# Performance work log

Measured on AMD Instinct MI355X. Metric: run time of the kernel, lower is better.

The kernel has to match this reference:

```python
import jax, jax.numpy as jnp
import numpy as np

BETA_MIN, BETA_MAX = 0.01, 0.995
EPS_DELTA, EPS_RMS = 1e-6, 1e-5


def _rmsnorm(x, w):
    ms = jnp.mean(x * x, axis=-1, keepdims=True)
    return x * jax.lax.rsqrt(ms + EPS_RMS) * w


def _delta_scan(q, k, v, beta, mask, bb1, bb2):
    # q, k, v: [B, S, D]; beta, mask: [B, S, 1]; bb1, bb2: scalars
    phi_q = jax.nn.elu(q) + 1.0
    phi_k = jax.nn.elu(k) + 1.0
    b1_base = jnp.clip(jax.nn.sigmoid(bb1), BETA_MIN, BETA_MAX)
    b2_base = jnp.clip(jax.nn.sigmoid(bb2), BETA_MIN, BETA_MAX)
    B, S, D = q.shape

    def step(carry, inp):
        H1, H2, Z1, Z2 = carry
        qt, kt, vt, bt, mt = inp  # qt/kt/vt: [B,D], bt/mt: [B,1]
        bin_t = jnp.clip(bt, BETA_MIN, BETA_MAX)
        b1 = jnp.clip(b1_base * bin_t, BETA_MIN, BETA_MAX)  # [B,1]
        b2 = jnp.clip(b2_base * bin_t, BETA_MIN, BETA_MAX)
        kv = jnp.einsum('bd,be->bde', kt, vt) * mt[:, :, None]  # [B,D,D]
        H1 = H1 * b1[:, :, None] + kv
        H2 = H2 * b2[:, :, None] + kv
        km = kt * mt
        Z1 = Z1 * b1 + km
        Z2 = Z2 * b2 + km
        num = jnp.einsum('bd,bde->be', qt, H1 + H2)
        den = jnp.maximum(jnp.sum(qt * (Z1 + Z2), axis=-1, keepdims=True), EPS_DELTA)
        return (H1, H2, Z1, Z2), num / den * mt

    init = (jnp.zeros((B, D, D), q.dtype), jnp.zeros((B, D, D), q.dtype),
            jnp.zeros((B, D), q.dtype), jnp.zeros((B, D), q.dtype))
    xs = tuple(a.swapaxes(0, 1) for a in (phi_q, phi_k, v, beta, mask))
    _, outs = jax.lax.scan(step, init, xs)
    return outs.swapaxes(0, 1)  # [B, S, D]


def setup_inputs() -> dict:
    key = jax.random.key(0)
    B, S, Dm, H = 4, 2048, 512, 8
    ks = jax.random.split(key, 8)
    scale = float(1.0 / np.sqrt(Dm))
    return {
        'x': jax.random.normal(ks[0], (B, S, Dm), jnp.float32),
        'mask': jnp.ones((B, S), jnp.float32),
        'Wq': jax.random.normal(ks[1], (Dm, Dm), jnp.float32) * scale,
        'Wk': jax.random.normal(ks[2], (Dm, Dm), jnp.float32) * scale,
        'Wv': jax.random.normal(ks[3], (Dm, Dm), jnp.float32) * scale,
        'Wb': jax.random.normal(ks[4], (H, Dm), jnp.float32) * scale,
        'bb': jnp.full((H,), 1.5, jnp.float32),
        'Wo': jax.random.normal(ks[5], (Dm, Dm), jnp.float32) * scale,
        'bo': jnp.zeros((Dm,), jnp.float32),
        'ln_w': jnp.ones((Dm,), jnp.float32),
        'recency': jnp.zeros((H,), jnp.float32),
        'base_beta_1': jnp.asarray(2.0, jnp.float32),
        'base_beta_2': jnp.asarray(3.0, jnp.float32),
    }


def reference(x, mask, Wq, Wk, Wv, Wb, bb, Wo, bo, ln_w, recency,
              base_beta_1, base_beta_2):
    B, S, Dm = x.shape
    H = recency.shape[0]
    d = Dm // H
    h = _rmsnorm(x, ln_w)
    q = h @ Wq.T
    k = h @ Wk.T
    v = h @ Wv.T
    # input-conditioned gate with per-head recency bias  -> [B, S, H]
    beta = jax.nn.sigmoid(h @ Wb.T + bb + recency)

    def to_heads(t):  # [B,S,Dm] -> [B*H, S, d]
        return t.reshape(B, S, H, d).transpose(0, 2, 1, 3).reshape(B * H, S, d)

    qh, kh, vh = to_heads(q), to_heads(k), to_heads(v)
    betah = beta.transpose(0, 2, 1).reshape(B * H, S, 1)
    maskh = jnp.broadcast_to(mask[:, None, :, None], (B, H, S, 1)).reshape(B * H, S, 1)
    o = _delta_scan(qh, kh, vh, betah, maskh, base_beta_1, base_beta_2)
    o = o.reshape(B, H, S, d).transpose(0, 2, 1, 3).reshape(B, S, Dm)
    return x + (o @ Wo.T + bo)
```

## Files before the change

kernel.cpp:

```cpp
#include <hip/hip_runtime.h>
#include <stdint.h>

typedef unsigned short u16;
typedef short bf16x8 __attribute__((ext_vector_type(8)));
typedef unsigned short u16x8 __attribute__((ext_vector_type(8)));
typedef unsigned short u16x4 __attribute__((ext_vector_type(4)));
typedef float f32x4 __attribute__((ext_vector_type(4)));

#define S_ 2048
#define DM 512
#define DH 64
#define CL 64
#define NCH 32

#define SW(r, sc) ((r) * 72 + ((sc) ^ (((r) & 7) << 3)))

__device__ __forceinline__ float b2f(u16 u) { return __uint_as_float(((unsigned)u) << 16); }
__device__ __forceinline__ u16 f2b(float f) {
    unsigned v = __float_as_uint(f);
    unsigned r = v + 0x7fffu + ((v >> 16) & 1u);
    return (u16)(r >> 16);
}
__device__ __forceinline__ float phi_elu(float x) { return x > 0.f ? x + 1.f : __expf(x); }
__device__ __forceinline__ float clip01(float v) { return fminf(fmaxf(v, 0.01f), 0.995f); }

__global__ __launch_bounds__(256) void k_rmsnorm(const float* __restrict__ x,
                                                 const float* __restrict__ lnw,
                                                 u16* __restrict__ h) {
    int wave = threadIdx.x >> 6, lane = threadIdx.x & 63;
    int row = blockIdx.x * 4 + wave;
    const float* xr = x + (size_t)row * DM + lane * 8;
    float4 v0 = *(const float4*)xr;
    float4 v1 = *(const float4*)(xr + 4);
    float ss = v0.x * v0.x + v0.y * v0.y + v0.z * v0.z + v0.w * v0.w +
               v1.x * v1.x + v1.y * v1.y + v1.z * v1.z + v1.w * v1.w;
    #pragma unroll
    for (int off = 32; off; off >>= 1) ss += __shfl_xor(ss, off, 64);
    float sc = rsqrtf(ss * (1.f / DM) + 1e-5f);
    const float* wr_ = lnw + lane * 8;
    float4 w0 = *(const float4*)wr_;
    float4 w1 = *(const float4*)(wr_ + 4);
    u16x8 o;
    o[0] = f2b(v0.x * sc * w0.x); o[1] = f2b(v0.y * sc * w0.y);
    o[2] = f2b(v0.z * sc * w0.z); o[3] = f2b(v0.w * sc * w0.w);
    o[4] = f2b(v1.x * sc * w1.x); o[5] = f2b(v1.y * sc * w1.y);
    o[6] = f2b(v1.z * sc * w1.z); o[7] = f2b(v1.w * sc * w1.w);
    *(u16x8*)(h + (size_t)row * DM + lane * 8) = o;
}

__global__ __launch_bounds__(256) void k_convw(const float* __restrict__ Wq, const float* __restrict__ Wk,
                                               const float* __restrict__ Wv, const float* __restrict__ Wo,
                                               u16* __restrict__ wcat, u16* __restrict__ wo) {
    int idx = blockIdx.x * 256 + threadIdx.x;
    int e0 = idx << 2;
    if (e0 < 1536 * 512) {
        int r = e0 >> 9, ccol = e0 & 511;
        const float* src = (r < 512) ? (Wq + (size_t)r * 512)
                         : (r < 1024) ? (Wk + (size_t)(r - 512) * 512)
                                      : (Wv + (size_t)(r - 1024) * 512);
        float4 v = *(const float4*)(src + ccol);
        u16x4 o = {f2b(v.x), f2b(v.y), f2b(v.z), f2b(v.w)};
        *(u16x4*)(wcat + e0) = o;
    } else {
        int e = e0 - 1536 * 512;
        float4 v = *(const float4*)(Wo + e);
        u16x4 o = {f2b(v.x), f2b(v.y), f2b(v.z), f2b(v.w)};
        *(u16x4*)(wo + e) = o;
    }
}

template<int MODE>
__global__ __launch_bounds__(256) void k_gemm(const u16* __restrict__ A, const u16* __restrict__ Bw, int K,
                                              const float* __restrict__ mask, u16* __restrict__ qh,
                                              u16* __restrict__ kh, u16* __restrict__ vh,
                                              const float* __restrict__ xres, const float* __restrict__ bo,
                                              float* __restrict__ outp) {
    __shared__ u16 As[128 * 40];
    __shared__ u16 Bs[128 * 40];
    int tid = threadIdx.x;
    int lane = tid & 63, wave = tid >> 6;
    int wr = wave >> 1, wc = wave & 1;
    int m0 = blockIdx.x * 128, n0 = blockIdx.y * 128;
    f32x4 acc[4][4] = {};
    int srow = tid >> 2, sc8 = (tid & 3) << 3;
    const u16* Ag0 = A + (size_t)(m0 + srow) * K + sc8;
    const u16* Ag1 = Ag0 + (size_t)64 * K;
    const u16* Bg0 = Bw + (size_t)(n0 + srow) * K + sc8;
    const u16* Bg1 = Bg0 + (size_t)64 * K;
    u16* As0 = &As[srow * 40 + sc8];
    u16* As1 = &As[(srow + 64) * 40 + sc8];
    u16* Bs0 = &Bs[srow * 40 + sc8];
    u16* Bs1 = &Bs[(srow + 64) * 40 + sc8];
    int kh8 = (lane >> 4) << 3;
    for (int k0 = 0; k0 < K; k0 += 32) {
        u16x8 a0 = *(const u16x8*)(Ag0 + k0);
        u16x8 a1 = *(const u16x8*)(Ag1 + k0);
        u16x8 b0 = *(const u16x8*)(Bg0 + k0);
        u16x8 b1 = *(const u16x8*)(Bg1 + k0);
        if (k0) __syncthreads();
        *(u16x8*)As0 = a0; *(u16x8*)As1 = a1;
        *(u16x8*)Bs0 = b0; *(u16x8*)Bs1 = b1;
        __syncthreads();
        bf16x8 af[4], bfr[4];
        #pragma unroll
        for (int m = 0; m < 4; m++) af[m] = *(const bf16x8*)&As[(wr * 64 + m * 16 + (lane & 15)) * 40 + kh8];
        #pragma unroll
        for (int n = 0; n < 4; n++) bfr[n] = *(const bf16x8*)&Bs[(wc * 64 + n * 16 + (lane & 15)) * 40 + kh8];
        #pragma unroll
        for (int m = 0; m < 4; m++)
            #pragma unroll
            for (int n = 0; n < 4; n++)
                acc[m][n] = __builtin_amdgcn_mfma_f32_16x16x32_bf16(af[m], bfr[n], acc[m][n], 0, 0, 0);
    }
    #pragma unroll
    for (int m = 0; m < 4; m++) {
        int rbase = m0 + wr * 64 + m * 16 + ((lane >> 4) << 2);
        #pragma unroll
        for (int n = 0; n < 4; n++) {
            int col = n0 + wc * 64 + n * 16 + (lane & 15);
            #pragma unroll
            for (int r = 0; r < 4; r++) {
                int row = rbase + r;
                float v = acc[m][n][r];
                if constexpr (MODE == 0) {
                    int mat = col >> 9, f = col & 511, hh = f >> 6, j = f & 63;
                    int b = row >> 11, s = row & 2047;
                    size_t di = ((size_t)((b << 3) + hh) * S_ + s) * DH + j;
                    if (mat == 0) qh[di] = f2b(phi_elu(v));
                    else if (mat == 1) kh[di] = f2b(phi_elu(v) * mask[(b << 11) + s]);
                    else vh[di] = f2b(v);
                } else {
                    size_t oi = (size_t)row * DM + col;
                    outp[oi] = v + xres[oi] + bo[col];
                }
            }
        }
    }
}

__global__ __launch_bounds__(256) void k_beta(const u16* __restrict__ h, const float* __restrict__ Wb,
                                              const float* __restrict__ bb, const float* __restrict__ rec,
                                              const float* __restrict__ bb1p, const float* __restrict__ bb2p,
                                              float* __restrict__ lb1, float* __restrict__ lb2) {
    int wave = threadIdx.x >> 6, lane = threadIdx.x & 63;
    int row = blockIdx.x * 4 + wave;
    const u16* hr = h + (size_t)row * DM + lane * 8;
    u16x8 hu = *(const u16x8*)hr;
    float hv[8];
    #pragma unroll
    for (int j = 0; j < 8; j++) hv[j] = b2f(hu[j]);
    float acc[8];
    #pragma unroll
    for (int hd = 0; hd < 8; hd++) {
        const float* wp = Wb + hd * DM + lane * 8;
        float4 w0 = *(const float4*)wp;
        float4 w1 = *(const float4*)(wp + 4);
        acc[hd] = hv[0] * w0.x + hv[1] * w0.y + hv[2] * w0.z + hv[3] * w0.w +
                  hv[4] * w1.x + hv[5] * w1.y + hv[6] * w1.z + hv[7] * w1.w;
    }
    #pragma unroll
    for (int hd = 0; hd < 8; hd++) {
        #pragma unroll
        for (int off = 32; off; off >>= 1) acc[hd] += __shfl_xor(acc[hd], off, 64);
    }
    if (lane == 0) {
        float b1b = clip01(1.f / (1.f + __expf(-bb1p[0])));
        float b2b = clip01(1.f / (1.f + __expf(-bb2p[0])));
        int b = row >> 11, s = row & 2047;
        #pragma unroll
        for (int hd = 0; hd < 8; hd++) {
            float logit = acc[hd] + bb[hd] + rec[hd];
            float beta = 1.f / (1.f + __expf(-logit));
            float bin = clip01(beta);
            float b1 = clip01(b1b * bin);
            float b2 = clip01(b2b * bin);
            size_t o = (size_t)((b << 3) + hd) * S_ + s;
            lb1[o] = log2f(b1);
            lb2[o] = log2f(b2);
        }
    }
}

__global__ __launch_bounds__(256) void k_pass1(const u16* __restrict__ kh, const u16* __restrict__ vh,
                                               const float* __restrict__ lb1, const float* __restrict__ lb2,
                                               float* __restrict__ S1, float* __restrict__ S2,
                                               float* __restrict__ z1, float* __restrict__ z2,
                                               float* __restrict__ P1, float* __restrict__ P2) {
    __shared__ u16 Kw1[64 * 72];
    __shared__ u16 Kw2[64 * 72];
    __shared__ u16 Vt[64 * 72];
    __shared__ float Ls1[64], Ls2[64];
    int tid = threadIdx.x;
    int bh = blockIdx.x >> 5, c = blockIdx.x & 31;
    int wave = tid >> 6, lane = tid & 63;
    size_t base = ((size_t)bh * S_ + c * CL) * DH;
    if (wave == 0) {
        float v = lb1[(size_t)bh * S_ + c * CL + lane];
        #pragma unroll
        for (int d = 1; d < 64; d <<= 1) { float o = __shfl_up(v, d, 64); if (lane >= d) v += o; }
        Ls1[lane] = v;
    } else if (wave == 1) {
        float v = lb2[(size_t)bh * S_ + c * CL + lane];
        #pragma unroll
        for (int d = 1; d < 64; d <<= 1) { float o = __shfl_up(v, d, 64); if (lane >= d) v += o; }
        Ls2[lane] = v;
    }
    int ss = tid & 63, i0 = (tid >> 6) << 4;
    const u16* kr = kh + base + (size_t)ss * DH + i0;
    u16x8 kk0 = *(const u16x8*)kr;
    u16x8 kk1 = *(const u16x8*)(kr + 8);
    {
        const u16* vr = vh + base + (size_t)ss * DH + i0;
        u16x8 vv0 = *(const u16x8*)vr;
        u16x8 vv1 = *(const u16x8*)(vr + 8);
        #pragma unroll
        for (int j = 0; j < 8; j++) {
            Vt[SW(i0 + j, ss)] = vv0[j];
            Vt[SW(i0 + 8 + j, ss)] = vv1[j];
        }
    }
    __syncthreads();
    float w1 = exp2f(Ls1[63] - Ls1[ss]);
    float w2 = exp2f(Ls2[63] - Ls2[ss]);
    #pragma unroll
    for (int j = 0; j < 8; j++) {
        float k0 = b2f(kk0[j]), k1 = b2f(kk1[j]);
        Kw1[SW(i0 + j, ss)] = f2b(w1 * k0);
        Kw2[SW(i0 + j, ss)] = f2b(w2 * k0);
        Kw1[SW(i0 + 8 + j, ss)] = f2b(w1 * k1);
        Kw2[SW(i0 + 8 + j, ss)] = f2b(w2 * k1);
    }
    if (tid == 0) { P1[blockIdx.x] = exp2f(Ls1[63]); P2[blockIdx.x] = exp2f(Ls2[63]); }
    __syncthreads();
    int l15 = lane & 15, kh8 = (lane >> 4) << 3;
    int j0 = wave << 4;
    bf16x8 vf0 = *(const bf16x8*)&Vt[SW(j0 + l15, kh8)];
    bf16x8 vf1 = *(const bf16x8*)&Vt[SW(j0 + l15, 32 + kh8)];
    f32x4 a1[4], a2[4];
    #pragma unroll
    for (int it = 0; it < 4; it++) { a1[it] = (f32x4){0,0,0,0}; a2[it] = (f32x4){0,0,0,0}; }
    #pragma unroll
    for (int it = 0; it < 4; it++) {
        int ir = (it << 4) + l15;
        bf16x8 b0 = *(const bf16x8*)&Kw1[SW(ir, kh8)];
        bf16x8 b1 = *(const bf16x8*)&Kw1[SW(ir, 32 + kh8)];
        a1[it] = __builtin_amdgcn_mfma_f32_16x16x32_bf16(vf0, b0, a1[it], 0, 0, 0);
        a1[it] = __builtin_amdgcn_mfma_f32_16x16x32_bf16(vf1, b1, a1[it], 0, 0, 0);
        bf16x8 c0 = *(const bf16x8*)&Kw2[SW(ir, kh8)];
        bf16x8 c1 = *(const bf16x8*)&Kw2[SW(ir, 32 + kh8)];
        a2[it] = __builtin_amdgcn_mfma_f32_16x16x32_bf16(vf0, c0, a2[it], 0, 0, 0);
        a2[it] = __builtin_amdgcn_mfma_f32_16x16x32_bf16(vf1, c1, a2[it], 0, 0, 0);
    }
    {
        int iz = tid >> 2, sg = tid & 3;
        u16x8 x0 = *(const u16x8*)&Kw1[SW(iz, sg << 4)];
        u16x8 x1 = *(const u16x8*)&Kw1[SW(iz, (sg << 4) + 8)];
        u16x8 y0 = *(const u16x8*)&Kw2[SW(iz, sg << 4)];
        u16x8 y1 = *(const u16x8*)&Kw2[SW(iz, (sg << 4) + 8)];
        float z1v = 0.f, z2v = 0.f;
        #pragma unroll
        for (int j = 0; j < 8; j++) {
            z1v += b2f(x0[j]) + b2f(x1[j]);
            z2v += b2f(y0[j]) + b2f(y1[j]);
        }
        z1v += __shfl_xor(z1v, 1, 64); z1v += __shfl_xor(z1v, 2, 64);
        z2v += __shfl_xor(z2v, 1, 64); z2v += __shfl_xor(z2v, 2, 64);
        if (sg == 0) {
            z1[(size_t)blockIdx.x * 64 + iz] = z1v;
            z2[(size_t)blockIdx.x * 64 + iz] = z2v;
        }
    }
    int jr0 = j0 + ((lane >> 4) << 2);
    #pragma unroll
    for (int it = 0; it < 4; it++) {
        int ii = (it << 4) + l15;
        #pragma unroll
        for (int r = 0; r < 4; r++) {
            size_t o = (size_t)blockIdx.x * 4096 + (size_t)(jr0 + r) * 64 + ii;
            S1[o] = a1[it][r];
            S2[o] = a2[it][r];
        }
    }
}

__global__ __launch_bounds__(256) void k_pass2(float* __restrict__ S1, float* __restrict__ S2,
                                               float* __restrict__ z1, float* __restrict__ z2,
                                               const float* __restrict__ P1, const float* __restrict__ P2) {
    int bh = blockIdx.x >> 4, part = blockIdx.x & 15;
    int e = part * 256 + threadIdx.x;
    float c1 = 0.f, c2 = 0.f;
    for (int c = 0; c < NCH; c++) {
        int bc = bh * NCH + c;
        size_t idx = (size_t)bc * 4096 + e;
        float p1 = P1[bc], p2 = P2[bc];
        float t1 = S1[idx]; S1[idx] = c1; c1 = c1 * p1 + t1;
        float t2 = S2[idx]; S2[idx] = c2; c2 = c2 * p2 + t2;
    }
    if (part == 0 && threadIdx.x < 64) {
        float y1 = 0.f, y2 = 0.f;
        for (int c = 0; c < NCH; c++) {
            int bc = bh * NCH + c;
            size_t zi = (size_t)bc * 64 + threadIdx.x;
            float p1 = P1[bc], p2 = P2[bc];
            float t1 = z1[zi]; z1[zi] = y1; y1 = y1 * p1 + t1;
            float t2 = z2[zi]; z2[zi] = y2; y2 = y2 * p2 + t2;
        }
    }
}

__global__ __launch_bounds__(256) void k_pass3(const u16* __restrict__ qh, const u16* __restrict__ kh,
                                               const u16* __restrict__ vh, const float* __restrict__ lb1,
                                               const float* __restrict__ lb2, const float* __restrict__ S1,
                                               const float* __restrict__ S2, const float* __restrict__ z1,
                                               const float* __restrict__ z2, const float* __restrict__ mask,
                                               u16* __restrict__ obf) {
    __shared__ u16 Vt[64 * 72];
    __shared__ u16 H1s[64 * 72];
    __shared__ u16 H2s[64 * 72];
    __shared__ u16 AWs[64 * 72];
    __shared__ float Ls1[64], Ls2[64], dens[64], qZ1[64], qZ2[64];
    int tid = threadIdx.x;
    int bh = blockIdx.x >> 5, c = blockIdx.x & 31;
    int wave = tid >> 6, lane = tid & 63;
    size_t base = ((size_t)bh * S_ + c * CL) * DH;
    if (wave == 0) {
        float v = lb1[(size_t)bh * S_ + c * CL + lane];
        #pragma unroll
        for (int d = 1; d < 64; d <<= 1) { float o = __shfl_up(v, d, 64); if (lane >= d) v += o; }
        Ls1[lane] = v;
    } else if (wave == 1) {
        float v = lb2[(size_t)bh * S_ + c * CL + lane];
        #pragma unroll
        for (int d = 1; d < 64; d <<= 1) { float o = __shfl_up(v, d, 64); if (lane >= d) v += o; }
        Ls2[lane] = v;
    }
    {
        int ss = tid & 63, i0 = (tid >> 6) << 4;
        const u16* vr = vh + base + (size_t)ss * DH + i0;
        u16x8 vv0 = *(const u16x8*)vr;
        u16x8 vv1 = *(const u16x8*)(vr + 8);
        #pragma unroll
        for (int j = 0; j < 8; j++) {
            Vt[SW(i0 + j, ss)] = vv0[j];
            Vt[SW(i0 + 8 + j, ss)] = vv1[j];
        }
    }
    {
        int j = tid >> 2, i04 = (tid & 3) << 4;
        const float* s1p = S1 + (size_t)blockIdx.x * 4096 + (size_t)j * 64 + i04;
        const float* s2p = S2 + (size_t)blockIdx.x * 4096 + (size_t)j * 64 + i04;
        float4 a0 = *(const float4*)s1p;
        float4 a1 = *(const float4*)(s1p + 4);
        float4 a2 = *(const float4*)(s1p + 8);
        float4 a3 = *(const float4*)(s1p + 12);
        u16x8 h0 = {f2b(a0.x), f2b(a0.y), f2b(a0.z), f2b(a0.w), f2b(a1.x), f2b(a1.y), f2b(a1.z), f2b(a1.w)};
        u16x8 h1 = {f2b(a2.x), f2b(a2.y), f2b(a2.z), f2b(a2.w), f2b(a3.x), f2b(a3.y), f2b(a3.z), f2b(a3.w)};
        *(u16x8*)&H1s[SW(j, i04)] = h0;
        *(u16x8*)&H1s[SW(j, i04 + 8)] = h1;
        float4 b0 = *(const float4*)s2p;
        float4 b1 = *(const float4*)(s2p + 4);
        float4 b2 = *(const float4*)(s2p + 8);
        float4 b3 = *(const float4*)(s2p + 12);
        u16x8 g0 = {f2b(b0.x), f2b(b0.y), f2b(b0.z), f2b(b0.w), f2b(b1.x), f2b(b1.y), f2b(b1.z), f2b(b1.w)};
        u16x8 g1 = {f2b(b2.x), f2b(b2.y), f2b(b2.z), f2b(b2.w), f2b(b3.x), f2b(b3.y), f2b(b3.z), f2b(b3.w)};
        *(u16x8*)&H2s[SW(j, i04)] = g0;
        *(u16x8*)&H2s[SW(j, i04 + 8)] = g1;
    }
    {
        int t = tid >> 2, g = tid & 3;
        const u16* qp = qh + base + (size_t)t * DH + (g << 4);
        u16x8 q0 = *(const u16x8*)qp;
        u16x8 q1 = *(const u16x8*)(qp + 8);
        const float* z1p = z1 + (size_t)blockIdx.x * 64 + (g << 4);
        const float* z2p = z2 + (size_t)blockIdx.x * 64 + (g << 4);
        float az1 = 0.f, az2 = 0.f;
        #pragma unroll
        for (int m = 0; m < 8; m++) {
            float qv0 = b2f(q0[m]), qv1 = b2f(q1[m]);
            az1 += qv0 * z1p[m] + qv1 * z1p[m + 8];
            az2 += qv0 * z2p[m] + qv1 * z2p[m + 8];
        }
        az1 += __shfl_xor(az1, 1, 64); az1 += __shfl_xor(az1, 2, 64);
        az2 += __shfl_xor(az2, 1, 64); az2 += __shfl_xor(az2, 2, 64);
        if (g == 0) { qZ1[t] = az1; qZ2[t] = az2; }
    }
    int l15 = lane & 15, kh8 = (lane >> 4) << 3;
    int t0 = wave << 4;
    const u16* qb = qh + base + (size_t)(t0 + l15) * DH;
    bf16x8 qf0 = *(const bf16x8*)(qb + kh8);
    bf16x8 qf1 = *(const bf16x8*)(qb + 32 + kh8);
    f32x4 accA[4];
    #pragma unroll
    for (int st = 0; st < 4; st++) accA[st] = (f32x4){0, 0, 0, 0};
    #pragma unroll
    for (int st = 0; st < 4; st++) {
        const u16* kb = kh + base + (size_t)((st << 4) + l15) * DH;
        bf16x8 kf0 = *(const bf16x8*)(kb + kh8);
        bf16x8 kf1 = *(const bf16x8*)(kb + 32 + kh8);
        accA[st] = __builtin_amdgcn_mfma_f32_16x16x32_bf16(qf0, kf0, accA[st], 0, 0, 0);
        accA[st] = __builtin_amdgcn_mfma_f32_16x16x32_bf16(qf1, kf1, accA[st], 0, 0, 0);
    }
    __syncthreads();
    int trow = t0 + ((lane >> 4) << 2);
    float l1t[4], l2t[4];
    #pragma unroll
    for (int r = 0; r < 4; r++) { l1t[r] = Ls1[trow + r]; l2t[r] = Ls2[trow + r]; }
    float rs[4] = {0.f, 0.f, 0.f, 0.f};
    #pragma unroll
    for (int st = 0; st < 4; st++) {
        int s = (st << 4) + l15;
        float s1 = Ls1[s], s2 = Ls2[s];
        #pragma unroll
        for (int r = 0; r < 4; r++) {
            float w = 0.f;
            if (s <= trow + r) w = exp2f(l1t[r] - s1) + exp2f(l2t[r] - s2);
            u16 awb = f2b(accA[st][r] * w);
            AWs[SW(trow + r, s)] = awb;
            rs[r] += b2f(awb);
        }
    }
    #pragma unroll
    for (int off = 1; off < 16; off <<= 1) {
        #pragma unroll
        for (int r = 0; r < 4; r++) rs[r] += __shfl_xor(rs[r], off, 64);
    }
    if (l15 == 0) {
        #pragma unroll
        for (int r = 0; r < 4; r++) dens[trow + r] = rs[r];
    }
    __syncthreads();
    bf16x8 awf0 = *(const bf16x8*)&AWs[SW(t0 + l15, kh8)];
    bf16x8 awf1 = *(const bf16x8*)&AWs[SW(t0 + l15, 32 + kh8)];
    f32x4 accO[4], accC1[4], accC2[4];
    #pragma unroll
    for (int jt = 0; jt < 4; jt++) {
        accO[jt] = (f32x4){0, 0, 0, 0};
        accC1[jt] = (f32x4){0, 0, 0, 0};
        accC2[jt] = (f32x4){0, 0, 0, 0};
    }
    #pragma unroll
    for (int jt = 0; jt < 4; jt++) {
        int jr = (jt << 4) + l15;
        bf16x8 v0 = *(const bf16x8*)&Vt[SW(jr, kh8)];
        bf16x8 v1 = *(const bf16x8*)&Vt[SW(jr, 32 + kh8)];
        accO[jt] = __builtin_amdgcn_mfma_f32_16x16x32_bf16(awf0, v0, accO[jt], 0, 0, 0);
        accO[jt] = __builtin_amdgcn_mfma_f32_16x16x32_bf16(awf1, v1, accO[jt], 0, 0, 0);
        bf16x8 h10 = *(const bf16x8*)&H1s[SW(jr, kh8)];
        bf16x8 h11 = *(const bf16x8*)&H1s[SW(jr, 32 + kh8)];
        accC1[jt] = __builtin_amdgcn_mfma_f32_16x16x32_bf16(qf0, h10, accC1[jt], 0, 0, 0);
        accC1[jt] = __builtin_amdgcn_mfma_f32_16x16x32_bf16(qf1, h11, accC1[jt], 0, 0, 0);
        bf16x8 h20 = *(const bf16x8*)&H2s[SW(jr, kh8)];
        bf16x8 h21 = *(const bf16x8*)&H2s[SW(jr, 32 + kh8)];
        accC2[jt] = __builtin_amdgcn_mfma_f32_16x16x32_bf16(qf0, h20, accC2[jt], 0, 0, 0);
        accC2[jt] = __builtin_amdgcn_mfma_f32_16x16x32_bf16(qf1, h21, accC2[jt], 0, 0, 0);
    }
    int b = bh >> 3, hh = bh & 7;
    #pragma unroll
    for (int r = 0; r < 4; r++) {
        int t = trow + r;
        float e1 = exp2f(l1t[r]), e2 = exp2f(l2t[r]);
        float den = dens[t] + e1 * qZ1[t] + e2 * qZ2[t];
        den = fmaxf(den, 1e-6f);
        int sg = (c << 6) + t;
        float mv = mask[(size_t)b * S_ + sg];
        float inv = mv / den;
        u16* op = obf + ((size_t)b * S_ + sg) * DM + hh * DH;
        #pragma unroll
        for (int jt = 0; jt < 4; jt++) {
            float numv = accO[jt][r] + e1 * accC1[jt][r] + e2 * accC2[jt][r];
            op[(jt << 4) + l15] = f2b(numv * inv);
        }
    }
}

extern "C" void kernel_launch(void* const* d_in, const int* in_sizes, int n_in,
                              void* d_out, int out_size, void* d_ws, size_t ws_size,
                              hipStream_t stream) {
    const float* x    = (const float*)d_in[0];
    const float* mask = (const float*)d_in[1];
    const float* Wq   = (const float*)d_in[2];
    const float* Wk   = (const float*)d_in[3];
    const float* Wv   = (const float*)d_in[4];
    const float* Wb   = (const float*)d_in[5];
    const float* bb   = (const float*)d_in[6];
    const float* Wo   = (const float*)d_in[7];
    const float* bo   = (const float*)d_in[8];
    const float* lnw  = (const float*)d_in[9];
    const float* rec  = (const float*)d_in[10];
    const float* bb1  = (const float*)d_in[11];
    const float* bb2  = (const float*)d_in[12];
    float* out = (float*)d_out;

    char* w = (char*)d_ws;
    u16* h    = (u16*)w;  w += (size_t)8192 * 512 * 2;
    u16* wcat = (u16*)w;  w += (size_t)1536 * 512 * 2;
    u16* wo   = (u16*)w;  w += (size_t)512 * 512 * 2;
    u16* qh   = (u16*)w;  w += (size_t)8192 * 512 * 2;
    u16* kh   = (u16*)w;  w += (size_t)8192 * 512 * 2;
    u16* vh   = (u16*)w;  w += (size_t)8192 * 512 * 2;
    float* lb1 = (float*)w; w += (size_t)32 * 2048 * 4;
    float* lb2 = (float*)w; w += (size_t)32 * 2048 * 4;
    float* S1  = (float*)w; w += (size_t)1024 * 4096 * 4;
    float* S2  = (float*)w; w += (size_t)1024 * 4096 * 4;
    float* z1  = (float*)w; w += (size_t)1024 * 64 * 4;
    float* z2  = (float*)w; w += (size_t)1024 * 64 * 4;
    float* P1  = (float*)w; w += 4096;
    float* P2  = (float*)w; w += 4096;
    u16* obf   = (u16*)w;   w += (size_t)8192 * 512 * 2;

    k_rmsnorm<<<2048, 256, 0, stream>>>(x, lnw, h);
    k_convw<<<1024, 256, 0, stream>>>(Wq, Wk, Wv, Wo, wcat, wo);
    k_gemm<0><<<dim3(64, 12), 256, 0, stream>>>(h, wcat, 512, mask, qh, kh, vh, nullptr, nullptr, nullptr);
    k_beta<<<2048, 256, 0, stream>>>(h, Wb, bb, rec, bb1, bb2, lb1, lb2);
    k_pass1<<<1024, 256, 0, stream>>>(kh, vh, lb1, lb2, S1, S2, z1, z2, P1, P2);
    k_pass2<<<512, 256, 0, stream>>>(S1, S2, z1, z2, P1, P2);
    k_pass3<<<1024, 256, 0, stream>>>(qh, kh, vh, lb1, lb2, S1, S2, z1, z2, mask, obf);
    k_gemm<1><<<dim3(64, 4), 256, 0, stream>>>(obf, wo, 512, nullptr, nullptr, nullptr, nullptr, x, bo, out);
}
```

Measured before the change: 121.1 us.

## Fuse beta into rmsnorm, store chunk states as bf16, use LDS-direct GEMM loads

Several changes at once. The beta-gate computation moves into the rmsnorm kernel, so h no longer has to be re-read and one launch goes away. The GEMM stages tiles with global_load_lds directly into unpadded LDS. The inter-chunk state S1/S2 is stored in bf16 instead of fp32, which halves traffic across pass1, pass2 and pass3. pass2 is vectorised to 8 elements per thread on 64 blocks, and pass3 reads the states straight from global memory instead of staging them in LDS. Risks: extra rounding in the state carry, bank conflicts in the unpadded GEMM LDS layout, and a pass2 grid of only 64 blocks that may underfill the GPU.

Result: no change. 118.9 us (-1.8%).

```diff
diff --git a/kernel.cpp b/kernel.cpp
--- a/kernel.cpp
+++ b/kernel.cpp
@@ -24,9 +24,16 @@
 __device__ __forceinline__ float phi_elu(float x) { return x > 0.f ? x + 1.f : __expf(x); }
 __device__ __forceinline__ float clip01(float v) { return fminf(fmaxf(v, 0.01f), 0.995f); }
 
-__global__ __launch_bounds__(256) void k_rmsnorm(const float* __restrict__ x,
-                                                 const float* __restrict__ lnw,
-                                                 u16* __restrict__ h) {
+__device__ __forceinline__ void gload16(const u16* g, u16* l) {
+    __builtin_amdgcn_global_load_lds((const __attribute__((address_space(1))) void*)g,
+                                     (__attribute__((address_space(3))) void*)l, 16, 0, 0);
+}
+
+__global__ __launch_bounds__(256) void k_rb(const float* __restrict__ x, const float* __restrict__ lnw,
+                                            const float* __restrict__ Wb, const float* __restrict__ bb,
+                                            const float* __restrict__ rec, const float* __restrict__ bb1p,
+                                            const float* __restrict__ bb2p, u16* __restrict__ h,
+                                            float* __restrict__ lb1, float* __restrict__ lb2) {
     int wave = threadIdx.x >> 6, lane = threadIdx.x & 63;
     int row = blockIdx.x * 4 + wave;
     const float* xr = x + (size_t)row * DM + lane * 8;
@@ -40,12 +47,45 @@
     const float* wr_ = lnw + lane * 8;
     float4 w0 = *(const float4*)wr_;
     float4 w1 = *(const float4*)(wr_ + 4);
+    float hv[8];
+    hv[0] = v0.x * sc * w0.x; hv[1] = v0.y * sc * w0.y;
+    hv[2] = v0.z * sc * w0.z; hv[3] = v0.w * sc * w0.w;
+    hv[4] = v1.x * sc * w1.x; hv[5] = v1.y * sc * w1.y;
+    hv[6] = v1.z * sc * w1.z; hv[7] = v1.w * sc * w1.w;
     u16x8 o;
-    o[0] = f2b(v0.x * sc * w0.x); o[1] = f2b(v0.y * sc * w0.y);
-    o[2] = f2b(v0.z * sc * w0.z); o[3] = f2b(v0.w * sc * w0.w);
-    o[4] = f2b(v1.x * sc * w1.x); o[5] = f2b(v1.y * sc * w1.y);
-    o[6] = f2b(v1.z * sc * w1.z); o[7] = f2b(v1.w * sc * w1.w);
+    #pragma unroll
+    for (int j = 0; j < 8; j++) o[j] = f2b(hv[j]);
     *(u16x8*)(h + (size_t)row * DM + lane * 8) = o;
+    float acc[8];
+    #pragma unroll
+    for (int hd = 0; hd < 8; hd++) {
+        const float* wp = Wb + hd * DM + lane * 8;
+        float4 a0 = *(const float4*)wp;
+        float4 a1 = *(const float4*)(wp + 4);
+        acc[hd] = hv[0] * a0.x + hv[1] * a0.y + hv[2] * a0.z + hv[3] * a0.w +
+                  hv[4] * a1.x + hv[5] * a1.y + hv[6] * a1.z + hv[7] * a1.w;
+    }
+    #pragma unroll
+    for (int hd = 0; hd < 8; hd++) {
+        #pragma unroll
+        for (int off = 32; off; off >>= 1) acc[hd] += __shfl_xor(acc[hd], off, 64);
+    }
+    if (lane == 0) {
+        float b1b = clip01(1.f / (1.f + __expf(-bb1p[0])));
+        float b2b = clip01(1.f / (1.f + __expf(-bb2p[0])));
+        int b = row >> 11, s = row & 2047;
+        #pragma unroll
+        for (int hd = 0; hd < 8; hd++) {
+            float logit = acc[hd] + bb[hd] + rec[hd];
+            float beta = 1.f / (1.f + __expf(-logit));
+            float bin = clip01(beta);
+            float b1 = clip01(b1b * bin);
+            float b2 = clip01(b2b * bin);
+            size_t o2 = (size_t)((b << 3) + hd) * S_ + s;
+            lb1[o2] = log2f(b1);
+            lb2[o2] = log2f(b2);
+        }
+    }
 }
 
 __global__ __launch_bounds__(256) void k_convw(const float* __restrict__ Wq, const float* __restrict__ Wk,
@@ -75,37 +115,36 @@
                                               u16* __restrict__ kh, u16* __restrict__ vh,
                                               const float* __restrict__ xres, const float* __restrict__ bo,
                                               float* __restrict__ outp) {
-    __shared__ u16 As[128 * 40];
-    __shared__ u16 Bs[128 * 40];
+    __shared__ u16 As[128 * 32];
+    __shared__ u16 Bs[128 * 32];
     int tid = threadIdx.x;
-    int lane = tid & 63, wave = tid >> 6;
-    int wr = wave >> 1, wc = wave & 1;
+    int lane = tid & 63, w = tid >> 6;
+    int wr = w >> 1, wc = w & 1;
     int m0 = blockIdx.x * 128, n0 = blockIdx.y * 128;
     f32x4 acc[4][4] = {};
-    int srow = tid >> 2, sc8 = (tid & 3) << 3;
-    const u16* Ag0 = A + (size_t)(m0 + srow) * K + sc8;
-    const u16* Ag1 = Ag0 + (size_t)64 * K;
-    const u16* Bg0 = Bw + (size_t)(n0 + srow) * K + sc8;
-    const u16* Bg1 = Bg0 + (size_t)64 * K;
-    u16* As0 = &As[srow * 40 + sc8];
-    u16* As1 = &As[(srow + 64) * 40 + sc8];
-    u16* Bs0 = &Bs[srow * 40 + sc8];
-    u16* Bs1 = &Bs[(srow + 64) * 40 + sc8];
-    int kh8 = (lane >> 4) << 3;
+    int srow = w * 32 + (lane >> 2);
+    int skel = (lane & 3) << 3;
+    const u16* gA0 = A + (size_t)(m0 + srow) * K + skel;
+    const u16* gA1 = gA0 + (size_t)16 * K;
+    const u16* gB0 = Bw + (size_t)(n0 + srow) * K + skel;
+    const u16* gB1 = gB0 + (size_t)16 * K;
+    u16* lA0 = &As[(w * 32) * 32];
+    u16* lA1 = &As[(w * 32 + 16) * 32];
+    u16* lB0 = &Bs[(w * 32) * 32];
+    u16* lB1 = &Bs[(w * 32 + 16) * 32];
+    int l15 = lane & 15, kh8 = (lane >> 4) << 3;
     for (int k0 = 0; k0 < K; k0 += 32) {
-        u16x8 a0 = *(const u16x8*)(Ag0 + k0);
-        u16x8 a1 = *(const u16x8*)(Ag1 + k0);
-        u16x8 b0 = *(const u16x8*)(Bg0 + k0);
-        u16x8 b1 = *(const u16x8*)(Bg1 + k0);
         if (k0) __syncthreads();
-        *(u16x8*)As0 = a0; *(u16x8*)As1 = a1;
-        *(u16x8*)Bs0 = b0; *(u16x8*)Bs1 = b1;
+        gload16(gA0 + k0, lA0);
+        gload16(gA1 + k0, lA1);
+        gload16(gB0 + k0, lB0);
+        gload16(gB1 + k0, lB1);
         __syncthreads();
         bf16x8 af[4], bfr[4];
         #pragma unroll
-        for (int m = 0; m < 4; m++) af[m] = *(const bf16x8*)&As[(wr * 64 + m * 16 + (lane & 15)) * 40 + kh8];
-        #pragma unroll
-        for (int n = 0; n < 4; n++) bfr[n] = *(const bf16x8*)&Bs[(wc * 64 + n * 16 + (lane & 15)) * 40 + kh8];
+        for (int m = 0; m < 4; m++) af[m] = *(const bf16x8*)&As[(wr * 64 + m * 16 + l15) * 32 + kh8];
+        #pragma unroll
+        for (int n = 0; n < 4; n++) bfr[n] = *(const bf16x8*)&Bs[(wc * 64 + n * 16 + l15) * 32 + kh8];
         #pragma unroll
         for (int m = 0; m < 4; m++)
             #pragma unroll
@@ -117,7 +156,7 @@
         int rbase = m0 + wr * 64 + m * 16 + ((lane >> 4) << 2);
         #pragma unroll
         for (int n = 0; n < 4; n++) {
-            int col = n0 + wc * 64 + n * 16 + (lane & 15);
+            int col = n0 + wc * 64 + n * 16 + l15;
             #pragma unroll
             for (int r = 0; r < 4; r++) {
                 int row = rbase + r;
@@ -138,52 +177,9 @@
     }
 }
 
-__global__ __launch_bounds__(256) void k_beta(const u16* __restrict__ h, const float* __restrict__ Wb,
-                                              const float* __restrict__ bb, const float* __restrict__ rec,
-                                              const float* __restrict__ bb1p, const float* __restrict__ bb2p,
-                                              float* __restrict__ lb1, float* __restrict__ lb2) {
-    int wave = threadIdx.x >> 6, lane = threadIdx.x & 63;
-    int row = blockIdx.x * 4 + wave;
-    const u16* hr = h + (size_t)row * DM + lane * 8;
-    u16x8 hu = *(const u16x8*)hr;
-    float hv[8];
-    #pragma unroll
-    for (int j = 0; j < 8; j++) hv[j] = b2f(hu[j]);
-    float acc[8];
-    #pragma unroll
-    for (int hd = 0; hd < 8; hd++) {
-        const float* wp = Wb + hd * DM + lane * 8;
-        float4 w0 = *(const float4*)wp;
-        float4 w1 = *(const float4*)(wp + 4);
-        acc[hd] = hv[0] * w0.x + hv[1] * w0.y + hv[2] * w0.z + hv[3] * w0.w +
-                  hv[4] * w1.x + hv[5] * w1.y + hv[6] * w1.z + hv[7] * w1.w;
-    }
-    #pragma unroll
-    for (int hd = 0; hd < 8; hd++) {
-        #pragma unroll
-        for (int off = 32; off; off >>= 1) acc[hd] += __shfl_xor(acc[hd], off, 64);
-    }
-    if (lane == 0) {
-        float b1b = clip01(1.f / (1.f + __expf(-bb1p[0])));
-        float b2b = clip01(1.f / (1.f + __expf(-bb2p[0])));
-        int b = row >> 11, s = row & 2047;
-        #pragma unroll
-        for (int hd = 0; hd < 8; hd++) {
-            float logit = acc[hd] + bb[hd] + rec[hd];
-            float beta = 1.f / (1.f + __expf(-logit));
-            float bin = clip01(beta);
-            float b1 = clip01(b1b * bin);
-            float b2 = clip01(b2b * bin);
-            size_t o = (size_t)((b << 3) + hd) * S_ + s;
-            lb1[o] = log2f(b1);
-            lb2[o] = log2f(b2);
-        }
-    }
-}
-
 __global__ __launch_bounds__(256) void k_pass1(const u16* __restrict__ kh, const u16* __restrict__ vh,
                                                const float* __restrict__ lb1, const float* __restrict__ lb2,
-                                               float* __restrict__ S1, float* __restrict__ S2,
+                                               u16* __restrict__ S1b, u16* __restrict__ S2b,
                                                float* __restrict__ z1, float* __restrict__ z2,
                                                float* __restrict__ P1, float* __restrict__ P2) {
     __shared__ u16 Kw1[64 * 72];
@@ -271,30 +267,38 @@
         }
     }
     int jr0 = j0 + ((lane >> 4) << 2);
+    size_t so = (size_t)blockIdx.x * 4096;
     #pragma unroll
     for (int it = 0; it < 4; it++) {
         int ii = (it << 4) + l15;
         #pragma unroll
         for (int r = 0; r < 4; r++) {
-            size_t o = (size_t)blockIdx.x * 4096 + (size_t)(jr0 + r) * 64 + ii;
-            S1[o] = a1[it][r];
-            S2[o] = a2[it][r];
-        }
-    }
-}
-
-__global__ __launch_bounds__(256) void k_pass2(float* __restrict__ S1, float* __restrict__ S2,
+            S1b[so + (size_t)(jr0 + r) * 64 + ii] = f2b(a1[it][r]);
+            S2b[so + (size_t)(jr0 + r) * 64 + ii] = f2b(a2[it][r]);
+        }
+    }
+}
+
+__global__ __launch_bounds__(256) void k_pass2(u16* __restrict__ S1b, u16* __restrict__ S2b,
                                                float* __restrict__ z1, float* __restrict__ z2,
                                                const float* __restrict__ P1, const float* __restrict__ P2) {
-    int bh = blockIdx.x >> 4, part = blockIdx.x & 15;
-    int e = part * 256 + threadIdx.x;
-    float c1 = 0.f, c2 = 0.f;
+    int bh = blockIdx.x >> 1, part = blockIdx.x & 1;
+    int e0 = (part * 256 + threadIdx.x) * 8;
+    float c1[8] = {}, c2[8] = {};
     for (int c = 0; c < NCH; c++) {
         int bc = bh * NCH + c;
-        size_t idx = (size_t)bc * 4096 + e;
+        size_t idx = (size_t)bc * 4096 + e0;
+        u16x8 s1 = *(const u16x8*)&S1b[idx];
+        u16x8 s2 = *(const u16x8*)&S2b[idx];
         float p1 = P1[bc], p2 = P2[bc];
-        float t1 = S1[idx]; S1[idx] = c1; c1 = c1 * p1 + t1;
-        float t2 = S2[idx]; S2[idx] = c2; c2 = c2 * p2 + t2;
+        u16x8 o1, o2;
+        #pragma unroll
+        for (int j = 0; j < 8; j++) {
+            o1[j] = f2b(c1[j]); c1[j] = c1[j] * p1 + b2f(s1[j]);
+            o2[j] = f2b(c2[j]); c2[j] = c2[j] * p2 + b2f(s2[j]);
+        }
+        *(u16x8*)&S1b[idx] = o1;
+        *(u16x8*)&S2b[idx] = o2;
     }
     if (part == 0 && threadIdx.x < 64) {
         float y1 = 0.f, y2 = 0.f;
@@ -310,13 +314,11 @@
 
 __global__ __launch_bounds__(256) void k_pass3(const u16* __restrict__ qh, const u16* __restrict__ kh,
                                                const u16* __restrict__ vh, const float* __restrict__ lb1,
-                                               const float* __restrict__ lb2, const float* __restrict__ S1,
-                                               const float* __restrict__ S2, const float* __restrict__ z1,
+                                               const float* __restrict__ lb2, const u16* __restrict__ S1b,
+                                               const u16* __restrict__ S2b, const float* __restrict__ z1,
                                                const float* __restrict__ z2, const float* __restrict__ mask,
                                                u16* __restrict__ obf) {
     __shared__ u16 Vt[64 * 72];
-    __shared__ u16 H1s[64 * 72];
-    __shared__ u16 H2s[64 * 72];
     __shared__ u16 AWs[64 * 72];
     __shared__ float Ls1[64], Ls2[64], dens[64], qZ1[64], qZ2[64];
     int tid = threadIdx.x;
@@ -346,27 +348,6 @@
         }
     }
     {
-        int j = tid >> 2, i04 = (tid & 3) << 4;
-        const float* s1p = S1 + (size_t)blockIdx.x * 4096 + (size_t)j * 64 + i04;
-        const float* s2p = S2 + (size_t)blockIdx.x * 4096 + (size_t)j * 64 + i04;
-        float4 a0 = *(const float4*)s1p;
-        float4 a1 = *(const float4*)(s1p + 4);
-        float4 a2 = *(const float4*)(s1p + 8);
-        float4 a3 = *(const float4*)(s1p + 12);
-        u16x8 h0 = {f2b(a0.x), f2b(a0.y), f2b(a0.z), f2b(a0.w), f2b(a1.x), f2b(a1.y), f2b(a1.z), f2b(a1.w)};
-        u16x8 h1 = {f2b(a2.x), f2b(a2.y), f2b(a2.z), f2b(a2.w), f2b(a3.x), f2b(a3.y), f2b(a3.z), f2b(a3.w)};
-        *(u16x8*)&H1s[SW(j, i04)] = h0;
-        *(u16x8*)&H1s[SW(j, i04 + 8)] = h1;
-        float4 b0 = *(const float4*)s2p;
-        float4 b1 = *(const float4*)(s2p + 4);
-        float4 b2 = *(const float4*)(s2p + 8);
-        float4 b3 = *(const float4*)(s2p + 12);
-        u16x8 g0 = {f2b(b0.x), f2b(b0.y), f2b(b0.z), f2b(b0.w), f2b(b1.x), f2b(b1.y), f2b(b1.z), f2b(b1.w)};
-        u16x8 g1 = {f2b(b2.x), f2b(b2.y), f2b(b2.z), f2b(b2.w), f2b(b3.x), f2b(b3.y), f2b(b3.z), f2b(b3.w)};
-        *(u16x8*)&H2s[SW(j, i04)] = g0;
-        *(u16x8*)&H2s[SW(j, i04 + 8)] = g1;
-    }
-    {
         int t = tid >> 2, g = tid & 3;
         const u16* qp = qh + base + (size_t)t * DH + (g << 4);
         u16x8 q0 = *(const u16x8*)qp;
@@ -431,6 +412,8 @@
     __syncthreads();
     bf16x8 awf0 = *(const bf16x8*)&AWs[SW(t0 + l15, kh8)];
     bf16x8 awf1 = *(const bf16x8*)&AWs[SW(t0 + l15, 32 + kh8)];
+    const u16* h1g = S1b + (size_t)blockIdx.x * 4096;
+    const u16* h2g = S2b + (size_t)blockIdx.x * 4096;
     f32x4 accO[4], accC1[4], accC2[4];
     #pragma unroll
     for (int jt = 0; jt < 4; jt++) {
@@ -445,12 +428,12 @@
         bf16x8 v1 = *(const bf16x8*)&Vt[SW(jr, 32 + kh8)];
         accO[jt] = __builtin_amdgcn_mfma_f32_16x16x32_bf16(awf0, v0, accO[jt], 0, 0, 0);
         accO[jt] = __builtin_amdgcn_mfma_f32_16x16x32_bf16(awf1, v1, accO[jt], 0, 0, 0);
-        bf16x8 h10 = *(const bf16x8*)&H1s[SW(jr, kh8)];
-        bf16x8 h11 = *(const bf16x8*)&H1s[SW(jr, 32 + kh8)];
+        bf16x8 h10 = *(const bf16x8*)(h1g + (size_t)jr * 64 + kh8);
+        bf16x8 h11 = *(const bf16x8*)(h1g + (size_t)jr * 64 + 32 + kh8);
         accC1[jt] = __builtin_amdgcn_mfma_f32_16x16x32_bf16(qf0, h10, accC1[jt], 0, 0, 0);
         accC1[jt] = __builtin_amdgcn_mfma_f32_16x16x32_bf16(qf1, h11, accC1[jt], 0, 0, 0);
-        bf16x8 h20 = *(const bf16x8*)&H2s[SW(jr, kh8)];
-        bf16x8 h21 = *(const bf16x8*)&H2s[SW(jr, 32 + kh8)];
+        bf16x8 h20 = *(const bf16x8*)(h2g + (size_t)jr * 64 + kh8);
+        bf16x8 h21 = *(const bf16x8*)(h2g + (size_t)jr * 64 + 32 + kh8);
         accC2[jt] = __builtin_amdgcn_mfma_f32_16x16x32_bf16(qf0, h20, accC2[jt], 0, 0, 0);
         accC2[jt] = __builtin_amdgcn_mfma_f32_16x16x32_bf16(qf1, h21, accC2[jt], 0, 0, 0);
     }
@@ -500,20 +483,19 @@
     u16* vh   = (u16*)w;  w += (size_t)8192 * 512 * 2;
     float* lb1 = (float*)w; w += (size_t)32 * 2048 * 4;
     float* lb2 = (float*)w; w += (size_t)32 * 2048 * 4;
-    float* S1  = (float*)w; w += (size_t)1024 * 4096 * 4;
-    float* S2  = (float*)w; w += (size_t)1024 * 4096 * 4;
+    u16* S1b  = (u16*)w;  w += (size_t)1024 * 4096 * 2;
+    u16* S2b  = (u16*)w;  w += (size_t)1024 * 4096 * 2;
     float* z1  = (float*)w; w += (size_t)1024 * 64 * 4;
     float* z2  = (float*)w; w += (size_t)1024 * 64 * 4;
     float* P1  = (float*)w; w += 4096;
     float* P2  = (float*)w; w += 4096;
     u16* obf   = (u16*)w;   w += (size_t)8192 * 512 * 2;
 
-    k_rmsnorm<<<2048, 256, 0, stream>>>(x, lnw, h);
+    k_rb<<<2048, 256, 0, stream>>>(x, lnw, Wb, bb, rec, bb1, bb2, h, lb1, lb2);
     k_convw<<<1024, 256, 0, stream>>>(Wq, Wk, Wv, Wo, wcat, wo);
     k_gemm<0><<<dim3(64, 12), 256, 0, stream>>>(h, wcat, 512, mask, qh, kh, vh, nullptr, nullptr, nullptr);
-    k_beta<<<2048, 256, 0, stream>>>(h, Wb, bb, rec, bb1, bb2, lb1, lb2);
-    k_pass1<<<1024, 256, 0, stream>>>(kh, vh, lb1, lb2, S1, S2, z1, z2, P1, P2);
-    k_pass2<<<512, 256, 0, stream>>>(S1, S2, z1, z2, P1, P2);
-    k_pass3<<<1024, 256, 0, stream>>>(qh, kh, vh, lb1, lb2, S1, S2, z1, z2, mask, obf);
+    k_pass1<<<1024, 256, 0, stream>>>(kh, vh, lb1, lb2, S1b, S2b, z1, z2, P1, P2);
+    k_pass2<<<64, 256, 0, stream>>>(S1b, S2b, z1, z2, P1, P2);
+    k_pass3<<<1024, 256, 0, stream>>>(qh, kh, vh, lb1, lb2, S1b, S2b, z1, z2, mask, obf);
     k_gemm<1><<<dim3(64, 4), 256, 0, stream>>>(obf, wo, 512, nullptr, nullptr, nullptr, nullptr, x, bo, out);
 }
```
